# Performance work log

Measured on AMD Instinct MI355X. Metric: run time of the kernel, lower is better.

## Reference

```python
import jax, jax.numpy as jnp
import numpy as np

B, T, D, DU, H = 2048, 100, 128, 128, 128  # batch, seq_len, emb_dim, user_emb_dim, hidden (=emb_dim)


def _mlp(x, layers, act):
    for W, b in layers:
        x = act(x @ W.T + b)
    return x


def setup_inputs() -> dict:
    key = jax.random.key(0)
    ks = iter(jax.random.split(key, 48))
    def p(shape, scale=0.05):
        return jax.random.normal(next(ks), shape, jnp.float32) * scale
    lengths = jax.random.randint(next(ks), (B,), 1, T + 1).astype(jnp.int32)
    mask = (jnp.arange(T)[None, :] < lengths[:, None]).astype(jnp.int32)
    inp = {
        'user_embedding': p((B, DU), 1.0),
        'item_historical_embedding': p((B, T, D), 1.0),
        'item_embedding': p((B, D), 1.0),
        'mask': mask,
        'sequential_length': lengths,
        'gru_Wih': p((3 * H, D)), 'gru_Whh': p((3 * H, H)),
        'gru_bih': p((3 * H,)), 'gru_bhh': p((3 * H,)),
        'aug_Wr': p((H, D + H)), 'aug_br': p((H,)),
        'aug_Wu': p((H, D + H)), 'aug_bu': p((H,)),
        'aug_Wh': p((H, D + H)), 'aug_bh': p((H,)),
    }
    att_dims = [4 * D, 80, 40, 1]
    ph_dims = [4 * D + DU, 200, 80, 1]
    for i, (di, do) in enumerate(zip(att_dims[:-1], att_dims[1:])):
        inp['att_W%d' % i] = p((do, di)); inp['att_b%d' % i] = p((do,))
    for i, (di, do) in enumerate(zip(ph_dims[:-1], ph_dims[1:])):
        inp['ph_W%d' % i] = p((do, di)); inp['ph_b%d' % i] = p((do,))
    return inp


def _forward(mask, sequential_length, user_embedding, item_historical_embedding, item_embedding,
             gru_Wih, gru_Whh, gru_bih, gru_bhh,
             att_W0, att_b0, att_W1, att_b1, att_W2, att_b2,
             aug_Wr, aug_br, aug_Wu, aug_bu, aug_Wh, aug_bh,
             ph_W0, ph_b0, ph_W1, ph_b1, ph_W2, ph_b2):
    fmask = mask.astype(jnp.float32)
    hist_sum = (item_historical_embedding * fmask[:, :, None]).sum(1)
    hist_sum = hist_sum / sequential_length[:, None].astype(jnp.float32)  # (B, D)

    # standard GRU over time (torch nn.GRU gate math) via lax.scan
    def gru_step(h, x_t):
        gi = x_t @ gru_Wih.T + gru_bih
        gh = h @ gru_Whh.T + gru_bhh
        i_r, i_z, i_n = jnp.split(gi, 3, axis=-1)
        h_r, h_z, h_n = jnp.split(gh, 3, axis=-1)
        r = jax.nn.sigmoid(i_r + h_r)
        z = jax.nn.sigmoid(i_z + h_z)
        n = jnp.tanh(i_n + r * h_n)
        h_new = (1.0 - z) * n + z * h
        return h_new, h_new
    h0 = jnp.zeros((item_historical_embedding.shape[0], H), jnp.float32)
    _, gru_seq = jax.lax.scan(gru_step, h0, jnp.swapaxes(item_historical_embedding, 0, 1))
    keys = jnp.swapaxes(gru_seq, 0, 1)  # (B, T, H)

    # DIN-style activation unit (all-ReLU MLP since act='relu'), masked softmax over time
    q = jnp.broadcast_to(item_embedding[:, None, :], keys.shape)
    feat = jnp.concatenate([keys, q, keys - q, q * keys], axis=-1)  # (B, T, 4H)
    score = _mlp(feat, [(att_W0, att_b0), (att_W1, att_b1), (att_W2, att_b2)], jax.nn.relu)
    score = jnp.where(mask[:, :, None] == 1, score, -jnp.inf)
    attn = jax.nn.softmax(score, axis=1)[..., 0]  # (B, T)
    # return_score=False in source: pooled context vector is (mis)used as attention scores
    pooled = jnp.einsum('bt,btd->bd', attn, keys)  # (B, H)

    # AUGRU; source indexes pooled[:, t] as per-step attention score (requires T <= H)
    att_seq = pooled.T[:T]  # (T, B)
    def augru_step(h, inp):
        x_t, a_t = inp
        ti = jnp.concatenate([h, x_t], axis=-1)
        r = jax.nn.sigmoid(ti @ aug_Wr.T + aug_br)
        u = jax.nn.sigmoid(ti @ aug_Wu.T + aug_bu)
        h_hat = jnp.tanh(jnp.concatenate([h * r, x_t], axis=-1) @ aug_Wh.T + aug_bh)
        u = a_t[:, None] * u
        h_new = (1.0 - u) * h + u * h_hat
        return h_new, h_new
    _, aug_seq = jax.lax.scan(augru_step, h0, (jnp.swapaxes(keys, 0, 1), att_seq))
    aug_out = jnp.swapaxes(aug_seq, 0, 1)  # (B, T, H)

    idx = (sequential_length - 1).astype(jnp.int32)[:, None, None]
    attention_feature = jnp.take_along_axis(aug_out, idx, axis=1)[:, 0, :]  # (B, H)

    comb = jnp.concatenate([user_embedding, item_embedding, hist_sum,
                            item_embedding * hist_sum, attention_feature], axis=1)
    # PredictHead: all layers sigmoid (source's i != len(dims)-1 is always True)
    scores = _mlp(comb, [(ph_W0, ph_b0), (ph_W1, ph_b1), (ph_W2, ph_b2)], jax.nn.sigmoid)
    return scores[:, 0]


def reference(user_embedding, item_historical_embedding, item_embedding, mask, sequential_length,
              gru_Wih, gru_Whh, gru_bih, gru_bhh,
              att_W0, att_b0, att_W1, att_b1, att_W2, att_b2,
              aug_Wr, aug_br, aug_Wu, aug_bu, aug_Wh, aug_bh,
              ph_W0, ph_b0, ph_W1, ph_b1, ph_W2, ph_b2):
    return _forward(mask, sequential_length, user_embedding, item_historical_embedding, item_embedding,
                    gru_Wih, gru_Whh, gru_bih, gru_bhh,
                    att_W0, att_b0, att_W1, att_b1, att_W2, att_b2,
                    aug_Wr, aug_br, aug_Wu, aug_bu, aug_Wh, aug_bh,
                    ph_W0, ph_b0, ph_W1, ph_b1, ph_W2, ph_b2)
```

## Files before the change

### kernel.cpp

```cpp
#include <hip/hip_runtime.h>
#include <math.h>

#define BB 2048
#define TT 100
#define DD 128
#define HH 128

typedef __attribute__((ext_vector_type(8))) short bf16x8;
typedef __attribute__((ext_vector_type(4))) float f32x4;

__device__ __forceinline__ float sigm(float x) {
    return __builtin_amdgcn_rcpf(1.f + __expf(-x));
}
__device__ __forceinline__ float tanh_fast(float x) {
    x = fminf(fmaxf(x, -15.f), 15.f);
    float e = __expf(2.f * x);
    return (e - 1.f) * __builtin_amdgcn_rcpf(e + 1.f);
}
__device__ __forceinline__ short f2bf(float f) {
    union { float f; unsigned u; } v; v.f = f;
    unsigned r = v.u + 0x7FFF + ((v.u >> 16) & 1);
    return (short)(r >> 16);
}
__device__ __forceinline__ float bf2f(ushort u) {
    union { unsigned u; float f; } v; v.u = ((unsigned)u) << 16;
    return v.f;
}

#define RD_A(buf, kk) (*(const bf16x8*)((const char*)(buf) + arow * 256 + (((kk) * 64 + akg * 16) ^ ((arow & 7) << 4))))
#define ST_A(buf, row, c, val) (*(short*)((char*)(buf) + (row) * 256 + (((c) * 2) ^ (((row) & 7) << 4))) = (val))

__global__ void k_prep(const float* __restrict__ attW0,
                       float* __restrict__ Wk, float* __restrict__ Wd, float* __restrict__ WqmC) {
    int i = blockIdx.x * 256 + threadIdx.x;
    if (i < 128 * 80) {
        int d = i / 80, j = i - d * 80;
        Wk[i]   = attW0[j * 512 + d] + attW0[j * 512 + 256 + d];
        Wd[i]   = attW0[j * 512 + 384 + d];
        WqmC[i] = attW0[j * 512 + 128 + d] - attW0[j * 512 + 256 + d];
    }
}

__global__ void k_pack(const float* __restrict__ Wih, const float* __restrict__ Whh,
                       const float* __restrict__ Wr, const float* __restrict__ Wu, const float* __restrict__ Wh,
                       const float* __restrict__ attW1,
                       const float* __restrict__ phW0, const float* __restrict__ phW1,
                       ushort* __restrict__ Pgru, ushort* __restrict__ Pa1, ushort* __restrict__ Pa2,
                       ushort* __restrict__ W1bf, ushort* __restrict__ W0h, ushort* __restrict__ W1h) {
    int n = blockIdx.x * 256 + threadIdx.x;
    if (n < 98304) {
        int tile = n >> 11, kt = (n >> 9) & 3, li = (n >> 3) & 63, e = n & 7;
        int k = kt * 32 + (li >> 4) * 8 + e;
        float s;
        if (tile < 24) { int j = tile * 16 + (li & 15); s = Wih[j * 128 + k]; }
        else           { int j = (tile - 24) * 16 + (li & 15); s = Whh[j * 128 + k]; }
        Pgru[n] = (ushort)f2bf(s);
    }
    if (n < 65536) {
        int tile = n >> 12, kt = (n >> 9) & 7, li = (n >> 3) & 63, e = n & 7;
        int k = kt * 32 + (li >> 4) * 8 + e;
        int jj = tile * 16 + (li & 15);
        float s = (jj < 128) ? Wr[jj * 256 + k] : Wu[(jj - 128) * 256 + k];
        Pa1[n] = (ushort)f2bf(s);
    }
    if (n < 32768) {
        int tile = n >> 12, kt = (n >> 9) & 7, li = (n >> 3) & 63, e = n & 7;
        int k = kt * 32 + (li >> 4) * 8 + e;
        int j = tile * 16 + (li & 15);
        Pa2[n] = (ushort)f2bf(Wh[j * 256 + k]);
    }
    if (n < 4608) {
        int g = n >> 9;
        int nt = g / 3, kt = g - nt * 3;
        int li = (n >> 3) & 63, e = n & 7;
        int k = kt * 32 + (li >> 4) * 8 + e;
        int j2 = nt * 16 + (li & 15);
        float s = (k < 80 && j2 < 40) ? attW1[j2 * 80 + k] : 0.f;
        W1bf[n] = (ushort)f2bf(s);
    }
    if (n < 133120) {
        int g = n >> 9;
        int nt = g / 20, kt = g - nt * 20;
        int li = (n >> 3) & 63, e = n & 7;
        int k = kt * 32 + (li >> 4) * 8 + e;
        int j = nt * 16 + (li & 15);
        W0h[n] = (ushort)f2bf((j < 200) ? phW0[j * 640 + k] : 0.f);
    }
    if (n < 17920) {
        int g = n >> 9;
        int nt = g / 7, kt = g - nt * 7;
        int li = (n >> 3) & 63, e = n & 7;
        int k = kt * 32 + (li >> 4) * 8 + e;
        int j = nt * 16 + (li & 15);
        W1h[n] = (ushort)f2bf((k < 200 && j < 80) ? phW1[j * 200 + k] : 0.f);
    }
}

__global__ void k_weffbf(const float* __restrict__ item, const float* __restrict__ Wk,
                         const float* __restrict__ Wd, const float* __restrict__ WqmC,
                         const float* __restrict__ attb0,
                         ushort* __restrict__ Weffbf, float* __restrict__ bias2) {
    int b = blockIdx.x, tid = threadIdx.x;
    __shared__ float q[128];
    if (tid < 128) q[tid] = item[b * 128 + tid];
    __syncthreads();
    ushort* Wb = Weffbf + (size_t)b * 10240;
    for (int idx = tid; idx < 10240; idx += 256) {
        int e = idx & 7, li = (idx >> 3) & 63, kt = (idx >> 9) & 3, nt = idx >> 11;
        int d = kt * 32 + (li >> 4) * 8 + e;
        int j = nt * 16 + (li & 15);
        Wb[idx] = (ushort)f2bf(Wk[d * 80 + j] + q[d] * Wd[d * 80 + j]);
    }
    if (tid < 80) {
        float s = attb0[tid];
        for (int d = 0; d < 128; ++d) s += q[d] * WqmC[d * 80 + tid];
        bias2[b * 80 + tid] = s;
    }
}

__global__ __launch_bounds__(512) void k_gru_mfma(const float* __restrict__ hist,
                                                  const ushort* __restrict__ Wp,
                                                  const float* __restrict__ bih, const float* __restrict__ bhh,
                                                  const int* __restrict__ len,
                                                  ushort* __restrict__ keysbf, float* __restrict__ hsum) {
    int tid = threadIdx.x;
    int lane = tid & 63, w = tid >> 6;
    int b0 = blockIdx.x * 8;

    __shared__ ushort xbf[2][16 * 128];
    __shared__ ushort hbf[2][16 * 128];
    __shared__ int    ln_s[8];

    for (int e = tid; e < 16 * 128; e += 512) { xbf[0][e] = 0; xbf[1][e] = 0; hbf[0][e] = 0; hbf[1][e] = 0; }
    if (tid < 8) ln_s[tid] = len[b0 + tid];

    const bf16x8* Wv = (const bf16x8*)Wp;
    bf16x8 bfx[3][4], bfh[3][4];
#pragma unroll
    for (int g = 0; g < 3; ++g)
#pragma unroll
        for (int kt = 0; kt < 4; ++kt) {
            bfx[g][kt] = Wv[((g * 8 + w) * 4 + kt) * 64 + lane];
            bfh[g][kt] = Wv[(((24 + g * 8 + w)) * 4 + kt) * 64 + lane];
        }

    int arow = lane & 15, akg = lane >> 4;
    int c = w * 16 + arow;
    float birq = bih[c] + bhh[c];
    float bizq = bih[128 + c] + bhh[128 + c];
    float bin  = bih[256 + c];
    float bqn  = bhh[256 + c];
    float hold[4] = {0.f, 0.f, 0.f, 0.f};

    int srow = tid >> 6, sd0 = (tid & 63) * 2;
    const float* hsrc = &hist[(size_t)(b0 + srow) * TT * DD + sd0];
    float2 v = *(const float2*)hsrc;
    __syncthreads();
    int Lrow = ln_s[srow];
    float sum0 = 0.f, sum1 = 0.f;
    {
        unsigned pv = (unsigned)(unsigned short)f2bf(v.x) | ((unsigned)(unsigned short)f2bf(v.y) << 16);
        *(unsigned*)((char*)xbf[0] + srow * 256 + ((sd0 * 2) ^ ((srow & 7) << 4))) = pv;
        if (0 < Lrow) { sum0 += v.x; sum1 += v.y; }
        if (TT > 1) v = *(const float2*)(hsrc + DD);
    }
    __syncthreads();

    f32x4 accr, accz, accnx;
    {
        bf16x8 af[4];
#pragma unroll
        for (int kt = 0; kt < 4; ++kt) af[kt] = RD_A(xbf[0], kt);
        accr = (f32x4){0.f,0.f,0.f,0.f}; accz = accr; accnx = accr;
#pragma unroll
        for (int kt = 0; kt < 4; ++kt) {
            accr  = __builtin_amdgcn_mfma_f32_16x16x32_bf16(af[kt], bfx[0][kt], accr, 0, 0, 0);
            accz  = __builtin_amdgcn_mfma_f32_16x16x32_bf16(af[kt], bfx[1][kt], accz, 0, 0, 0);
            accnx = __builtin_amdgcn_mfma_f32_16x16x32_bf16(af[kt], bfx[2][kt], accnx, 0, 0, 0);
        }
    }

    int p = 0, q = 0;
    for (int t = 0; t < TT; ++t) {
        if (t + 1 < TT) {
            unsigned pv = (unsigned)(unsigned short)f2bf(v.x) | ((unsigned)(unsigned short)f2bf(v.y) << 16);
            *(unsigned*)((char*)xbf[p ^ 1] + srow * 256 + ((sd0 * 2) ^ ((srow & 7) << 4))) = pv;
            if (t + 1 < Lrow) { sum0 += v.x; sum1 += v.y; }
            if (t + 2 < TT) v = *(const float2*)(hsrc + (size_t)(t + 2) * DD);
        }

        bf16x8 ah[4];
#pragma unroll
        for (int kt = 0; kt < 4; ++kt) ah[kt] = RD_A(hbf[q], kt);
        f32x4 accnh = {0.f, 0.f, 0.f, 0.f};
#pragma unroll
        for (int kt = 0; kt < 4; ++kt) {
            accr  = __builtin_amdgcn_mfma_f32_16x16x32_bf16(ah[kt], bfh[0][kt], accr, 0, 0, 0);
            accz  = __builtin_amdgcn_mfma_f32_16x16x32_bf16(ah[kt], bfh[1][kt], accz, 0, 0, 0);
            accnh = __builtin_amdgcn_mfma_f32_16x16x32_bf16(ah[kt], bfh[2][kt], accnh, 0, 0, 0);
        }

        ushort* hw = (ushort*)hbf[q ^ 1];
#pragma unroll
        for (int i = 0; i < 4; ++i) {
            float r = sigm(accr[i] + birq);
            float z = sigm(accz[i] + bizq);
            float nn = tanh_fast(accnx[i] + bin + r * (accnh[i] + bqn));
            float hnew = (1.f - z) * nn + z * hold[i];
            hold[i] = hnew;
            if (akg < 2) {
                int row = akg * 4 + i;
                short hb16 = f2bf(hnew);
                ST_A(hw, row, c, hb16);
                keysbf[((size_t)(b0 + row) * TT + t) * HH + c] = (ushort)hb16;
            }
        }
        __syncthreads();

        if (t + 1 < TT) {
            bf16x8 af[4];
#pragma unroll
            for (int kt = 0; kt < 4; ++kt) af[kt] = RD_A(xbf[p ^ 1], kt);
            f32x4 ar = {0.f,0.f,0.f,0.f}, az = ar, an = ar;
#pragma unroll
            for (int kt = 0; kt < 4; ++kt) {
                ar = __builtin_amdgcn_mfma_f32_16x16x32_bf16(af[kt], bfx[0][kt], ar, 0, 0, 0);
                az = __builtin_amdgcn_mfma_f32_16x16x32_bf16(af[kt], bfx[1][kt], az, 0, 0, 0);
                an = __builtin_amdgcn_mfma_f32_16x16x32_bf16(af[kt], bfx[2][kt], an, 0, 0, 0);
            }
            accr = ar; accz = az; accnx = an;
        }
        p ^= 1; q ^= 1;
    }

    hsum[(b0 + srow) * 128 + sd0]     = sum0 / (float)Lrow;
    hsum[(b0 + srow) * 128 + sd0 + 1] = sum1 / (float)Lrow;
}

__global__ __launch_bounds__(512) void k_attnsoft(const ushort* __restrict__ keysbf,
                                                  const ushort* __restrict__ Weffbf,
                                                  const float* __restrict__ bias2,
                                                  const ushort* __restrict__ W1bf,
                                                  const float* __restrict__ attb1, const float* __restrict__ attW2,
                                                  const float* __restrict__ attb2,
                                                  const int* __restrict__ len,
                                                  float* __restrict__ pooled) {
    int tid = threadIdx.x;
    int lane = tid & 63, w = tid >> 6;
    int b = blockIdx.x;

    __shared__ ushort kbf[112 * 128];
    __shared__ ushort scbf[112 * 96];
    __shared__ float  bias2s[80];
    __shared__ float  b1s[48];
    __shared__ float  W2s[48];
    __shared__ float  attn_s[128];
    __shared__ float  red[128];
    __shared__ float  pred[512];

    bf16x8 bfrag0[5][4];
    bf16x8 bfrag1[3][3];
    if (w < 7) {
        const bf16x8* Wb = (const bf16x8*)(Weffbf + (size_t)b * 10240);
#pragma unroll
        for (int nt = 0; nt < 5; ++nt)
#pragma unroll
            for (int kt = 0; kt < 4; ++kt)
                bfrag0[nt][kt] = Wb[(nt * 4 + kt) * 64 + lane];
#pragma unroll
        for (int nt = 0; nt < 3; ++nt)
#pragma unroll
            for (int kt = 0; kt < 3; ++kt)
                bfrag1[nt][kt] = ((const bf16x8*)W1bf)[(nt * 3 + kt) * 64 + lane];
    }

    const ushort* ksrc = keysbf + (size_t)b * TT * 128;
    for (int e = tid; e < 3584; e += 512) {
        int row = e >> 5, c4 = e & 31;
        uint2 pv;
        if (row < TT) pv = *(const uint2*)(ksrc + row * 128 + c4 * 4);
        else { pv.x = 0; pv.y = 0; }
        *(uint2*)((char*)kbf + row * 256 + ((c4 * 8) ^ ((row & 7) << 4))) = pv;
    }
    for (int e = tid; e < 1792; e += 512) {
        int row = e >> 4, c = 80 + (e & 15);
        *(ushort*)((char*)scbf + row * 192 + ((c * 2) ^ ((row & 7) << 4))) = 0;
    }
    if (tid < 80) bias2s[tid] = bias2[b * 80 + tid];
    if (tid < 48) {
        b1s[tid] = (tid < 40) ? attb1[tid] : 0.f;
        W2s[tid] = (tid < 40) ? attW2[tid] : 0.f;
    }
    __syncthreads();

    if (w < 7) {
        int arow = lane & 15, akg = lane >> 4;
        int row = w * 16 + arow;
        bf16x8 af[4];
#pragma unroll
        for (int kt = 0; kt < 4; ++kt)
            af[kt] = *(const bf16x8*)((const char*)kbf + row * 256 + (((kt * 64 + akg * 16)) ^ ((row & 7) << 4)));
#pragma unroll
        for (int nt = 0; nt < 5; ++nt) {
            f32x4 acc = {0.f, 0.f, 0.f, 0.f};
#pragma unroll
            for (int kt = 0; kt < 4; ++kt)
                acc = __builtin_amdgcn_mfma_f32_16x16x32_bf16(af[kt], bfrag0[nt][kt], acc, 0, 0, 0);
            int col = nt * 16 + arow;
            float bcol = bias2s[col];
#pragma unroll
            for (int i = 0; i < 4; ++i) {
                int r2 = w * 16 + akg * 4 + i;
                float vsc = fmaxf(acc[i] + bcol, 0.f);
                *(short*)((char*)scbf + r2 * 192 + ((col * 2) ^ ((r2 & 7) << 4))) = f2bf(vsc);
            }
        }
    }
    __syncthreads();

    if (w < 7) {
        int arow = lane & 15, akg = lane >> 4;
        int row = w * 16 + arow;
        bf16x8 a1[3];
#pragma unroll
        for (int kt = 0; kt < 3; ++kt)
            a1[kt] = *(const bf16x8*)((const char*)scbf + row * 192 + (((kt * 64 + akg * 16)) ^ ((row & 7) << 4)));
        float pi[4] = {0.f, 0.f, 0.f, 0.f};
#pragma unroll
        for (int nt = 0; nt < 3; ++nt) {
            f32x4 acc = {0.f, 0.f, 0.f, 0.f};
#pragma unroll
            for (int kt = 0; kt < 3; ++kt)
                acc = __builtin_amdgcn_mfma_f32_16x16x32_bf16(a1[kt], bfrag1[nt][kt], acc, 0, 0, 0);
            int col = nt * 16 + arow;
            float wb = W2s[col], bb1 = b1s[col];
#pragma unroll
            for (int i = 0; i < 4; ++i)
                pi[i] += fmaxf(acc[i] + bb1, 0.f) * wb;
        }
#pragma unroll
        for (int off = 1; off < 16; off <<= 1)
#pragma unroll
            for (int i = 0; i < 4; ++i)
                pi[i] += __shfl_xor(pi[i], off);
        if ((lane & 15) == 0) {
            float b2 = attb2[0];
#pragma unroll
            for (int i = 0; i < 4; ++i) {
                int t = w * 16 + akg * 4 + i;
                if (t < 128) attn_s[t] = fmaxf(pi[i] + b2, 0.f);
            }
        }
    }
    __syncthreads();

    int L = len[b];
    if (tid < 128) red[tid] = (tid < L) ? attn_s[tid] : -INFINITY;
    __syncthreads();
    for (int o = 64; o >= 1; o >>= 1) { if (tid < o) red[tid] = fmaxf(red[tid], red[tid + o]); __syncthreads(); }
    float mx = red[0];
    __syncthreads();
    if (tid < 128) {
        float e = (tid < L) ? __expf(attn_s[tid] - mx) : 0.f;
        attn_s[tid] = e; red[tid] = e;
    }
    __syncthreads();
    for (int o = 64; o >= 1; o >>= 1) { if (tid < o) red[tid] += red[tid + o]; __syncthreads(); }
    float inv = __builtin_amdgcn_rcpf(red[0]);
    {
        int d = tid & 127, qd = tid >> 7;
        float p = 0.f;
        for (int t2 = qd; t2 < L; t2 += 4) {
            ushort kv = *(const ushort*)((const char*)kbf + t2 * 256 + ((d * 2) ^ ((t2 & 7) << 4)));
            p += attn_s[t2] * bf2f(kv);
        }
        pred[tid] = p;
    }
    __syncthreads();
    if (tid < 128)
        pooled[b * 128 + tid] = (pred[tid] + pred[128 + tid] + pred[256 + tid] + pred[384 + tid]) * inv;
}

__global__ __launch_bounds__(512) void k_augru_mfma(const ushort* __restrict__ keysbf,
                                                    const float* __restrict__ pooled,
                                                    const int* __restrict__ len,
                                                    const ushort* __restrict__ Wp1, const ushort* __restrict__ Wp2,
                                                    const float* __restrict__ br, const float* __restrict__ bu,
                                                    const float* __restrict__ bh,
                                                    float* __restrict__ att_feat) {
    int tid = threadIdx.x;
    int lane = tid & 63, w = tid >> 6;
    int b0 = blockIdx.x * 8;

    __shared__ ushort hbf[16 * 128], rhbf[16 * 128];
    __shared__ float as_[16];
    __shared__ int ln_s[8];

    for (int e = tid; e < 16 * 128; e += 512) { hbf[e] = 0; rhbf[e] = 0; }
    if (tid < 16) as_[tid] = 0.f;
    if (tid < 8) ln_s[tid] = len[b0 + tid];

    const bf16x8* W1v = (const bf16x8*)Wp1;
    const bf16x8* W2v = (const bf16x8*)Wp2;
    bf16x8 b1r[8], b1u[8], b2[8];
#pragma unroll
    for (int kt = 0; kt < 8; ++kt) {
        b1r[kt] = W1v[(w * 8 + kt) * 64 + lane];
        b1u[kt] = W1v[((8 + w) * 8 + kt) * 64 + lane];
        b2[kt]  = W2v[(w * 8 + kt) * 64 + lane];
    }

    int arow = lane & 15, akg = lane >> 4;
    int c = w * 16 + arow;
    float brc = br[c], buc = bu[c], bhc = bh[c];
    float hold[4] = {0.f, 0.f, 0.f, 0.f};

    int rowg = b0 + arow; if (rowg > BB - 1) rowg = BB - 1;
    const ushort* xbase = keysbf + (size_t)rowg * TT * HH + akg * 8;

    bf16x8 axc[4], axn[4];
#pragma unroll
    for (int kt = 0; kt < 4; ++kt) axc[kt] = *(const bf16x8*)(xbase + kt * 32);
    float areg = (tid < 8) ? pooled[(b0 + tid) * HH + 0] : 0.f;
    if (tid < 8) as_[tid] = areg;
    float aregn = (tid < 8 && TT > 1) ? pooled[(b0 + tid) * HH + 1] : 0.f;
    __syncthreads();

    f32x4 accr = {0.f,0.f,0.f,0.f}, accu = {0.f,0.f,0.f,0.f};
#pragma unroll
    for (int kt = 0; kt < 4; ++kt) {
        accr = __builtin_amdgcn_mfma_f32_16x16x32_bf16(axc[kt], b1r[4 + kt], accr, 0, 0, 0);
        accu = __builtin_amdgcn_mfma_f32_16x16x32_bf16(axc[kt], b1u[4 + kt], accu, 0, 0, 0);
    }

    for (int t = 0; t < TT; ++t) {
        if (t + 1 < TT) {
#pragma unroll
            for (int kt = 0; kt < 4; ++kt) axn[kt] = *(const bf16x8*)(xbase + (size_t)(t + 1) * HH + kt * 32);
        }

        bf16x8 ah[4];
#pragma unroll
        for (int kt = 0; kt < 4; ++kt) ah[kt] = RD_A(hbf, kt);
        f32x4 acch = {0.f,0.f,0.f,0.f};
#pragma unroll
        for (int kt = 0; kt < 4; ++kt) {
            accr = __builtin_amdgcn_mfma_f32_16x16x32_bf16(ah[kt], b1r[kt], accr, 0, 0, 0);
            accu = __builtin_amdgcn_mfma_f32_16x16x32_bf16(ah[kt], b1u[kt], accu, 0, 0, 0);
            acch = __builtin_amdgcn_mfma_f32_16x16x32_bf16(axc[kt], b2[4 + kt], acch, 0, 0, 0);
        }

        float u_reg[4];
#pragma unroll
        for (int i = 0; i < 4; ++i) {
            float r = sigm(accr[i] + brc);
            u_reg[i] = as_[akg * 4 + i] * sigm(accu[i] + buc);
            if (akg < 2) ST_A(rhbf, akg * 4 + i, c, f2bf(r * hold[i]));
        }
        __syncthreads();

        bf16x8 arh[4];
#pragma unroll
        for (int kt = 0; kt < 4; ++kt) arh[kt] = RD_A(rhbf, kt);
        f32x4 accr2 = {0.f,0.f,0.f,0.f}, accu2 = {0.f,0.f,0.f,0.f};
#pragma unroll
        for (int kt = 0; kt < 4; ++kt) {
            acch = __builtin_amdgcn_mfma_f32_16x16x32_bf16(arh[kt], b2[kt], acch, 0, 0, 0);
            accr2 = __builtin_amdgcn_mfma_f32_16x16x32_bf16(axn[kt], b1r[4 + kt], accr2, 0, 0, 0);
            accu2 = __builtin_amdgcn_mfma_f32_16x16x32_bf16(axn[kt], b1u[4 + kt], accu2, 0, 0, 0);
        }

#pragma unroll
        for (int i = 0; i < 4; ++i) {
            float hhat = tanh_fast(acch[i] + bhc);
            float hnew = (1.f - u_reg[i]) * hold[i] + u_reg[i] * hhat;
            hold[i] = hnew;
            if (akg < 2) {
                int row = akg * 4 + i;
                ST_A(hbf, row, c, f2bf(hnew));
                if (t == ln_s[row] - 1) att_feat[(b0 + row) * HH + c] = hnew;
            }
        }
        if (tid < 8) as_[tid] = aregn;
        if (tid < 8 && t + 2 < TT) aregn = pooled[(b0 + tid) * HH + t + 2];
        __syncthreads();

        accr = accr2; accu = accu2;
#pragma unroll
        for (int kt = 0; kt < 4; ++kt) axc[kt] = axn[kt];
    }
}

__global__ __launch_bounds__(64) void k_head(const float* __restrict__ user, const float* __restrict__ item,
                                             const float* __restrict__ hsum, const float* __restrict__ attf,
                                             const ushort* __restrict__ W0h, const ushort* __restrict__ W1h,
                                             const float* __restrict__ phb0, const float* __restrict__ phb1,
                                             const float* __restrict__ phW2, const float* __restrict__ phb2,
                                             float* __restrict__ out) {
    int lane = threadIdx.x;
    int b0 = blockIdx.x * 16;
    __shared__ ushort xb[16 * 128];
    __shared__ ushort h1b[16 * 256];

    for (int e = lane; e < 4096; e += 64) h1b[e] = 0;

    int arow = lane & 15, akg = lane >> 4;
    f32x4 acc0[13];
#pragma unroll
    for (int nt = 0; nt < 13; ++nt) acc0[nt] = (f32x4){0.f, 0.f, 0.f, 0.f};

    for (int c = 0; c < 5; ++c) {
        for (int idx = lane; idx < 1024; idx += 64) {
            int row = idx >> 6, c2 = (idx & 63) * 2;
            int g = (b0 + row) * 128 + c2;
            float2 v;
            if (c == 0) v = *(const float2*)&user[g];
            else if (c == 1) v = *(const float2*)&item[g];
            else if (c == 2) v = *(const float2*)&hsum[g];
            else if (c == 3) { float2 a = *(const float2*)&item[g]; float2 h = *(const float2*)&hsum[g];
                               v.x = a.x * h.x; v.y = a.y * h.y; }
            else v = *(const float2*)&attf[g];
            unsigned pv = (unsigned)(unsigned short)f2bf(v.x) | ((unsigned)(unsigned short)f2bf(v.y) << 16);
            *(unsigned*)((char*)xb + row * 256 + ((c2 * 2) ^ ((row & 7) << 4))) = pv;
        }
        __syncthreads();
        bf16x8 af[4];
#pragma unroll
        for (int kt = 0; kt < 4; ++kt)
            af[kt] = *(const bf16x8*)((const char*)xb + arow * 256 + ((kt * 64 + akg * 16) ^ ((arow & 7) << 4)));
#pragma unroll
        for (int nt = 0; nt < 13; ++nt) {
#pragma unroll
            for (int kt = 0; kt < 4; ++kt) {
                int ktg = c * 4 + kt;
                bf16x8 bf = ((const bf16x8*)W0h)[(nt * 20 + ktg) * 64 + lane];
                acc0[nt] = __builtin_amdgcn_mfma_f32_16x16x32_bf16(af[kt], bf, acc0[nt], 0, 0, 0);
            }
        }
        __syncthreads();
    }

#pragma unroll
    for (int nt = 0; nt < 13; ++nt) {
        int col = nt * 16 + arow;
        if (col < 200) {
            float bb = phb0[col];
#pragma unroll
            for (int i = 0; i < 4; ++i) {
                int r2 = akg * 4 + i;
                *(short*)((char*)h1b + r2 * 512 + ((col * 2) ^ ((r2 & 7) << 4))) = f2bf(sigm(acc0[nt][i] + bb));
            }
        }
    }
    __syncthreads();

    bf16x8 a1[7];
#pragma unroll
    for (int kt = 0; kt < 7; ++kt)
        a1[kt] = *(const bf16x8*)((const char*)h1b + arow * 512 + ((kt * 64 + akg * 16) ^ ((arow & 7) << 4)));
    float pi[4] = {0.f, 0.f, 0.f, 0.f};
#pragma unroll
    for (int nt = 0; nt < 5; ++nt) {
        f32x4 acc = {0.f, 0.f, 0.f, 0.f};
#pragma unroll
        for (int kt = 0; kt < 7; ++kt)
            acc = __builtin_amdgcn_mfma_f32_16x16x32_bf16(a1[kt], ((const bf16x8*)W1h)[(nt * 7 + kt) * 64 + lane], acc, 0, 0, 0);
        int col = nt * 16 + arow;
        float b1 = phb1[col], w2v = phW2[col];
#pragma unroll
        for (int i = 0; i < 4; ++i)
            pi[i] += sigm(acc[i] + b1) * w2v;
    }
#pragma unroll
    for (int off = 1; off < 16; off <<= 1)
#pragma unroll
        for (int i = 0; i < 4; ++i)
            pi[i] += __shfl_xor(pi[i], off);
    if (arow == 0) {
        float b2 = phb2[0];
#pragma unroll
        for (int i = 0; i < 4; ++i)
            out[b0 + akg * 4 + i] = sigm(pi[i] + b2);
    }
}

extern "C" void kernel_launch(void* const* d_in, const int* in_sizes, int n_in,
                              void* d_out, int out_size, void* d_ws, size_t ws_size,
                              hipStream_t stream) {
    const float* user = (const float*)d_in[0];
    const float* hist = (const float*)d_in[1];
    const float* item = (const float*)d_in[2];
    const int* len = (const int*)d_in[4];
    const float* gWih = (const float*)d_in[5];
    const float* gWhh = (const float*)d_in[6];
    const float* gbih = (const float*)d_in[7];
    const float* gbhh = (const float*)d_in[8];
    const float* aWr = (const float*)d_in[9];
    const float* abr = (const float*)d_in[10];
    const float* aWu = (const float*)d_in[11];
    const float* abu = (const float*)d_in[12];
    const float* aWh = (const float*)d_in[13];
    const float* abh = (const float*)d_in[14];
    const float* attW0 = (const float*)d_in[15];
    const float* attb0 = (const float*)d_in[16];
    const float* attW1 = (const float*)d_in[17];
    const float* attb1 = (const float*)d_in[18];
    const float* attW2 = (const float*)d_in[19];
    const float* attb2 = (const float*)d_in[20];
    const float* phW0 = (const float*)d_in[21];
    const float* phb0 = (const float*)d_in[22];
    const float* phW1 = (const float*)d_in[23];
    const float* phb1 = (const float*)d_in[24];
    const float* phW2 = (const float*)d_in[25];
    const float* phb2 = (const float*)d_in[26];

    char* ws = (char*)d_ws;
    size_t off = 0;
    auto alloc = [&](size_t bytes) { char* p = ws + off; off += (bytes + 255) & ~(size_t)255; return p; };
    ushort* keysbf  = (ushort*)alloc((size_t)BB * TT * HH * 2);
    ushort* Weffbf  = (ushort*)alloc((size_t)BB * 10240 * 2);
    float* pooled   = (float*)alloc((size_t)BB * HH * 4);
    float* hsum     = (float*)alloc((size_t)BB * DD * 4);
    float* attf     = (float*)alloc((size_t)BB * HH * 4);
    float* Wk       = (float*)alloc(128 * 80 * 4);
    float* Wd       = (float*)alloc(128 * 80 * 4);
    float* WqmC     = (float*)alloc(128 * 80 * 4);
    float* bias2    = (float*)alloc((size_t)BB * 80 * 4);
    ushort* Pgru    = (ushort*)alloc(98304 * 2);
    ushort* Pa1     = (ushort*)alloc(65536 * 2);
    ushort* Pa2     = (ushort*)alloc(32768 * 2);
    ushort* W1bf    = (ushort*)alloc(4608 * 2);
    ushort* W0h     = (ushort*)alloc(133120 * 2);
    ushort* W1h     = (ushort*)alloc(17920 * 2);
    (void)in_sizes; (void)n_in; (void)out_size; (void)ws_size;

    k_prep<<<40, 256, 0, stream>>>(attW0, Wk, Wd, WqmC);
    k_pack<<<520, 256, 0, stream>>>(gWih, gWhh, aWr, aWu, aWh, attW1, phW0, phW1,
                                    Pgru, Pa1, Pa2, W1bf, W0h, W1h);
    k_weffbf<<<BB, 256, 0, stream>>>(item, Wk, Wd, WqmC, attb0, Weffbf, bias2);
    k_gru_mfma<<<256, 512, 0, stream>>>(hist, Pgru, gbih, gbhh, len, keysbf, hsum);
    k_attnsoft<<<BB, 512, 0, stream>>>(keysbf, Weffbf, bias2, W1bf, attb1, attW2, attb2, len, pooled);
    k_augru_mfma<<<256, 512, 0, stream>>>(keysbf, pooled, len, Pa1, Pa2, abr, abu, abh, attf);
    k_head<<<128, 64, 0, stream>>>(user, item, hsum, attf, W0h, W1h, phb0, phb1, phW2, phb2, (float*)d_out);
}
```

Baseline: 432.7 us.

## Stage AUGRU input rows through double-buffered swizzled LDS and precompute x-part of candidate

Instead of each lane loading its own bf16x8 A-fragments of the next timestep's keys straight from global memory (duplicated across the 8 waves), the block now cooperatively loads each timestep's 8x128 input tile once into a double-buffered, XOR-swizzled LDS buffer and reads MFMA fragments from there. It also moves the x-side contribution to the candidate gate into the next-step precompute, which shortens the serial path after the second barrier. This cuts redundant global traffic and register pressure, at the cost of extra LDS space and LDS reads per step.

```diff
diff --git a/kernel.cpp b/kernel.cpp
--- a/kernel.cpp
+++ b/kernel.cpp
@@ -393,10 +393,11 @@
     int b0 = blockIdx.x * 8;
 
     __shared__ ushort hbf[16 * 128], rhbf[16 * 128];
+    __shared__ ushort xbf[2][16 * 128];
     __shared__ float as_[16];
     __shared__ int ln_s[8];
 
-    for (int e = tid; e < 16 * 128; e += 512) { hbf[e] = 0; rhbf[e] = 0; }
+    for (int e = tid; e < 16 * 128; e += 512) { hbf[e] = 0; rhbf[e] = 0; xbf[0][e] = 0; xbf[1][e] = 0; }
     if (tid < 16) as_[tid] = 0.f;
     if (tid < 8) ln_s[tid] = len[b0 + tid];
 
@@ -415,39 +416,44 @@
     float brc = br[c], buc = bu[c], bhc = bh[c];
     float hold[4] = {0.f, 0.f, 0.f, 0.f};
 
-    int rowg = b0 + arow; if (rowg > BB - 1) rowg = BB - 1;
-    const ushort* xbase = keysbf + (size_t)rowg * TT * HH + akg * 8;
-
-    bf16x8 axc[4], axn[4];
-#pragma unroll
-    for (int kt = 0; kt < 4; ++kt) axc[kt] = *(const bf16x8*)(xbase + kt * 32);
+    int srow = tid >> 6, sd0 = (tid & 63) * 2;
+    const ushort* xsrc = &keysbf[(size_t)(b0 + srow) * TT * HH + sd0];
+    unsigned v0 = *(const unsigned*)xsrc;
     float areg = (tid < 8) ? pooled[(b0 + tid) * HH + 0] : 0.f;
+    __syncthreads();
+    *(unsigned*)((char*)xbf[0] + srow * 256 + ((sd0 * 2) ^ ((srow & 7) << 4))) = v0;
     if (tid < 8) as_[tid] = areg;
+    unsigned vnext = (TT > 1) ? *(const unsigned*)(xsrc + (size_t)1 * HH) : 0u;
     float aregn = (tid < 8 && TT > 1) ? pooled[(b0 + tid) * HH + 1] : 0.f;
     __syncthreads();
 
-    f32x4 accr = {0.f,0.f,0.f,0.f}, accu = {0.f,0.f,0.f,0.f};
-#pragma unroll
-    for (int kt = 0; kt < 4; ++kt) {
-        accr = __builtin_amdgcn_mfma_f32_16x16x32_bf16(axc[kt], b1r[4 + kt], accr, 0, 0, 0);
-        accu = __builtin_amdgcn_mfma_f32_16x16x32_bf16(axc[kt], b1u[4 + kt], accu, 0, 0, 0);
-    }
-
+    f32x4 accr = {0.f,0.f,0.f,0.f}, accu = {0.f,0.f,0.f,0.f}, acchx = {0.f,0.f,0.f,0.f};
+    {
+        bf16x8 af[4];
+#pragma unroll
+        for (int kt = 0; kt < 4; ++kt) af[kt] = RD_A(xbf[0], kt);
+#pragma unroll
+        for (int kt = 0; kt < 4; ++kt) {
+            accr  = __builtin_amdgcn_mfma_f32_16x16x32_bf16(af[kt], b1r[4 + kt], accr, 0, 0, 0);
+            accu  = __builtin_amdgcn_mfma_f32_16x16x32_bf16(af[kt], b1u[4 + kt], accu, 0, 0, 0);
+            acchx = __builtin_amdgcn_mfma_f32_16x16x32_bf16(af[kt], b2[4 + kt], acchx, 0, 0, 0);
+        }
+    }
+
+    int p = 0;
     for (int t = 0; t < TT; ++t) {
         if (t + 1 < TT) {
-#pragma unroll
-            for (int kt = 0; kt < 4; ++kt) axn[kt] = *(const bf16x8*)(xbase + (size_t)(t + 1) * HH + kt * 32);
+            *(unsigned*)((char*)xbf[p ^ 1] + srow * 256 + ((sd0 * 2) ^ ((srow & 7) << 4))) = vnext;
+            if (t + 2 < TT) vnext = *(const unsigned*)(xsrc + (size_t)(t + 2) * HH);
         }
 
         bf16x8 ah[4];
 #pragma unroll
         for (int kt = 0; kt < 4; ++kt) ah[kt] = RD_A(hbf, kt);
-        f32x4 acch = {0.f,0.f,0.f,0.f};
 #pragma unroll
         for (int kt = 0; kt < 4; ++kt) {
             accr = __builtin_amdgcn_mfma_f32_16x16x32_bf16(ah[kt], b1r[kt], accr, 0, 0, 0);
             accu = __builtin_amdgcn_mfma_f32_16x16x32_bf16(ah[kt], b1u[kt], accu, 0, 0, 0);
-            acch = __builtin_amdgcn_mfma_f32_16x16x32_bf16(axc[kt], b2[4 + kt], acch, 0, 0, 0);
         }
 
         float u_reg[4];
@@ -462,12 +468,21 @@
         bf16x8 arh[4];
 #pragma unroll
         for (int kt = 0; kt < 4; ++kt) arh[kt] = RD_A(rhbf, kt);
-        f32x4 accr2 = {0.f,0.f,0.f,0.f}, accu2 = {0.f,0.f,0.f,0.f};
-#pragma unroll
-        for (int kt = 0; kt < 4; ++kt) {
+        f32x4 acch = acchx;
+        f32x4 accr2 = {0.f,0.f,0.f,0.f}, accu2 = {0.f,0.f,0.f,0.f}, acchx2 = {0.f,0.f,0.f,0.f};
+#pragma unroll
+        for (int kt = 0; kt < 4; ++kt)
             acch = __builtin_amdgcn_mfma_f32_16x16x32_bf16(arh[kt], b2[kt], acch, 0, 0, 0);
-            accr2 = __builtin_amdgcn_mfma_f32_16x16x32_bf16(axn[kt], b1r[4 + kt], accr2, 0, 0, 0);
-            accu2 = __builtin_amdgcn_mfma_f32_16x16x32_bf16(axn[kt], b1u[4 + kt], accu2, 0, 0, 0);
+        if (t + 1 < TT) {
+            bf16x8 axn[4];
+#pragma unroll
+            for (int kt = 0; kt < 4; ++kt) axn[kt] = RD_A(xbf[p ^ 1], kt);
+#pragma unroll
+            for (int kt = 0; kt < 4; ++kt) {
+                accr2  = __builtin_amdgcn_mfma_f32_16x16x32_bf16(axn[kt], b1r[4 + kt], accr2, 0, 0, 0);
+                accu2  = __builtin_amdgcn_mfma_f32_16x16x32_bf16(axn[kt], b1u[4 + kt], accu2, 0, 0, 0);
+                acchx2 = __builtin_amdgcn_mfma_f32_16x16x32_bf16(axn[kt], b2[4 + kt], acchx2, 0, 0, 0);
+            }
         }
 
 #pragma unroll
@@ -485,9 +500,8 @@
         if (tid < 8 && t + 2 < TT) aregn = pooled[(b0 + tid) * HH + t + 2];
         __syncthreads();
 
-        accr = accr2; accu = accu2;
-#pragma unroll
-        for (int kt = 0; kt < 4; ++kt) axc[kt] = axn[kt];
+        accr = accr2; accu = accu2; acchx = acchx2;
+        p ^= 1;
     }
 }
 
```

New measurement: 401.2 us, median of 2. -7.3%, faster.
